# Kernel optimization log

Measured on AMD Instinct MI355X. Metric: run time of the kernel, lower is better.

The kernel has to match this reference:

```python
import jax, jax.numpy as jnp
import numpy as np

D_MODEL = 128
SEQ_LEN = 2048
WINDOW = 64
BATCH = 32


def setup_inputs() -> dict:
    key = jax.random.key(0)
    ks = jax.random.split(key, 6)
    scale = 1.0 / np.sqrt(D_MODEL)
    return {
        "x": jax.random.normal(ks[0], (BATCH, D_MODEL, SEQ_LEN), dtype=jnp.float32),
        "Wq": jax.random.normal(ks[1], (D_MODEL, D_MODEL), dtype=jnp.float32) * scale,
        "bq": jnp.zeros((D_MODEL,), dtype=jnp.float32),
        "Wk": jax.random.normal(ks[2], (D_MODEL, D_MODEL), dtype=jnp.float32) * scale,
        "bk": jnp.zeros((D_MODEL,), dtype=jnp.float32),
        "Wv": jax.random.normal(ks[3], (D_MODEL, D_MODEL), dtype=jnp.float32) * scale,
        "bv": jnp.zeros((D_MODEL,), dtype=jnp.float32),
        "Wo": jax.random.normal(ks[4], (D_MODEL, D_MODEL), dtype=jnp.float32) * scale,
        "bo": jnp.zeros((D_MODEL,), dtype=jnp.float32),
        "pos_bias": jax.random.normal(ks[5], (SEQ_LEN, SEQ_LEN), dtype=jnp.float32) * 0.02,
    }


def reference(x, Wq, bq, Wk, bk, Wv, bv, Wo, bo, pos_bias):
    # x: [N, C, L] -> [N, L, C]  (in_proj Rearrange)
    xt = jnp.swapaxes(x, 1, 2)
    L = xt.shape[1]

    q = xt @ Wq + bq  # [N, L, d]
    k = xt @ Wk + bk
    v = xt @ Wv + bv

    # AFT-Local positional bias: w_{t,t'} = pos_bias if |t-t'| < s else 0
    idx = jnp.arange(L)
    local_mask = (jnp.abs(idx[:, None] - idx[None, :]) < WINDOW).astype(xt.dtype)
    pb = pos_bias[:L, :L] * local_mask  # [L, L]

    # numerically stable exponentials (AFT paper / labml formulation)
    exp_k = jnp.exp(k - jnp.max(k, axis=1, keepdims=True))          # [N, L, d]
    exp_pb = jnp.exp(pb - jnp.max(pb, axis=1, keepdims=True))       # [L, L]

    num = jnp.einsum('ij,njd->nid', exp_pb, exp_k * v)  # [N, L, d]
    den = jnp.einsum('ij,njd->nid', exp_pb, exp_k)      # [N, L, d]

    y = jax.nn.sigmoid(q) * num / den
    out = y @ Wo + bo  # output projection

    # out_proj Rearrange: [N, L, C] -> [N, C, L]
    return jnp.swapaxes(out, 1, 2)
```

## Files before the change

### kernel.cpp

```cpp
#include <hip/hip_runtime.h>
#include <math.h>

#define NB 32
#define DM 128
#define SL 2048
#define WIN 64
#define NT  (SL / 16)
#define PADF 4
#define PADB 6
#define NTP (NT + PADF + PADB)
#define YST 132
#define NSEG 64

typedef __attribute__((ext_vector_type(8))) short bf16x8;
typedef __attribute__((ext_vector_type(8))) unsigned short u16x8;
typedef __attribute__((ext_vector_type(4))) float f32x4;

__device__ inline ushort bf16_rne(float f) {
    union { float f; unsigned u; } v; v.f = f;
    unsigned u = v.u;
    return (ushort)((u + 0x7FFFu + ((u >> 16) & 1u)) >> 16);
}
__device__ inline float bf16_to_f(ushort h) {
    union { unsigned u; float f; } v; v.u = ((unsigned)h) << 16;
    return v.f;
}
__device__ inline ushort bf16_hi_trunc(float f) {
    union { float f; unsigned u; } v; v.f = f;
    return (ushort)(v.u >> 16);
}


__global__ __launch_bounds__(512) void setup_kernel(
    const float* __restrict__ Wq, const float* __restrict__ Wk,
    const float* __restrict__ Wv, const float* __restrict__ Wo,
    const float* __restrict__ pos_bias,
    ushort* __restrict__ Wh, ushort* __restrict__ Wl,
    ushort* __restrict__ WB)
{
    const int b = blockIdx.x;
    const int tid = threadIdx.x;
    if (b < 128) {
        const int id = b;
        const int mat = id >> 5;
        const int ct = (id & 31) >> 2, ks = id & 3;
        const int lane = tid >> 3, j = tid & 7;
        const int k = ks * 32 + (lane >> 4) * 8 + j;
        const int col = ct * 16 + (lane & 15);
        const float* W = (mat == 0) ? Wq : ((mat == 1) ? Wk : ((mat == 2) ? Wv : Wo));
        float w = W[k * DM + col];
        ushort h = bf16_rne(w);
        Wh[(size_t)id * 512 + tid] = h;
        Wl[(size_t)id * 512 + tid] = bf16_rne(w - bf16_to_f(h));
    } else {
        const int idx = b - 128;
        const int it = idx >> 1;
        const int half = idx & 1;
        const int i0 = it * 16;
        const int tend = half * 1280 + 1280;
        for (int t = half * 1280 + tid; t < tend; t += 512) {
            const int ks = t >> 9;
            const int lane = (t >> 3) & 63;
            const int jj = t & 7;
            const int m = lane & 15;
            const int k = ks * 32 + ((lane >> 4) << 3) + jj;
            const int i = i0 + m;
            const int j = i0 - 64 + k;
            const int rel = k - 64 - m;
            float val = 0.f;
            if (rel > -WIN && rel < WIN && j >= 0 && j < SL)
                val = __expf(pos_bias[(size_t)i * SL + j]) - 1.f;
            WB[(size_t)it * 2560 + t] = bf16_rne(val);
        }
    }
}

__global__ __launch_bounds__(512, 6) void qkv_kernel(
    const float* __restrict__ x,
    const ushort* __restrict__ Wh, const ushort* __restrict__ Wl,
    const float* __restrict__ bq, const float* __restrict__ bk,
    const float* __restrict__ bv,
    ushort* __restrict__ sqh, ushort* __restrict__ ekTF, ushort* __restrict__ ekvTF,
    float* __restrict__ Pk, float* __restrict__ Pkv)
{
    __shared__ ushort Ah[32 * 128];
    __shared__ ushort Al[32 * 128];
    const int n = blockIdx.y, bx = blockIdx.x, l0 = bx * 32;
    const int tid = threadIdx.x;
    const int wave = tid >> 6;
    const int lane = tid & 63;

    if (bx < 10) {
        const int jt_p = (bx < PADF) ? bx : (NT + bx);
        const size_t zb = ((size_t)n * NTP + jt_p) * 2048 + (size_t)tid * 4;
        ushort4 z; z.x = 0; z.y = 0; z.z = 0; z.w = 0;
        *(ushort4*)&ekTF [zb] = z;
        *(ushort4*)&ekvTF[zb] = z;
    }

    {
        const int lo = tid & 31;
        const int cq = tid >> 5;
        const int l  = l0 + lo;
        const int c0 = cq * 8;
        float xv[8];
        #pragma unroll
        for (int u = 0; u < 8; ++u)
            xv[u] = x[((size_t)n * DM + c0 + u) * SL + l];
        u16x8 hv, lv;
        #pragma unroll
        for (int u = 0; u < 8; ++u) {
            const ushort h = bf16_hi_trunc(xv[u]);
            hv[u] = h;
            lv[u] = bf16_rne(xv[u] - bf16_to_f(h));
        }
        const int lt = lo >> 4, m = lo & 15;
        const int ks = cq >> 2, oct = cq & 3;
        const int idx = ((lt * 4 + ks) * 64 + oct * 16 + m) * 8;
        *(u16x8*)&Ah[idx] = hv;
        *(u16x8*)&Al[idx] = lv;
    }
    __syncthreads();

    const int dcol = lane & 15;
    const int d = wave * 16 + dcol;

    f32x4 acc[3][2];
    {
        const float b0 = bq[d], b1 = bk[d], b2 = bv[d];
        #pragma unroll
        for (int lt = 0; lt < 2; ++lt) {
            acc[0][lt] = (f32x4){b0, b0, b0, b0};
            acc[1][lt] = (f32x4){b1, b1, b1, b1};
            acc[2][lt] = (f32x4){b2, b2, b2, b2};
        }
    }

    const bf16x8* WhV = (const bf16x8*)Wh;
    const bf16x8* WlV = (const bf16x8*)Wl;
    #pragma unroll
    for (int ks = 0; ks < 4; ++ks) {
        bf16x8 bh[3], bl[3];
        #pragma unroll
        for (int m = 0; m < 3; ++m) {
            const int fi = ((m * 8 + wave) * 4 + ks) * 64 + lane;
            bh[m] = WhV[fi];
            bl[m] = WlV[fi];
        }
        #pragma unroll
        for (int lt = 0; lt < 2; ++lt) {
            const bf16x8 ah = *(const bf16x8*)&Ah[((lt * 4 + ks) * 64 + lane) * 8];
            const bf16x8 al = *(const bf16x8*)&Al[((lt * 4 + ks) * 64 + lane) * 8];
            #pragma unroll
            for (int m = 0; m < 3; ++m) {
                acc[m][lt] = __builtin_amdgcn_mfma_f32_16x16x32_bf16(
                    ah, bh[m], acc[m][lt], 0, 0, 0);
                acc[m][lt] = __builtin_amdgcn_mfma_f32_16x16x32_bf16(
                    al, bh[m], acc[m][lt], 0, 0, 0);
                acc[m][lt] = __builtin_amdgcn_mfma_f32_16x16x32_bf16(
                    ah, bl[m], acc[m][lt], 0, 0, 0);
            }
        }
    }

    const int lrow0 = (lane >> 4) * 4;
    float psk = 0.f, pskv = 0.f;
    #pragma unroll
    for (int lt = 0; lt < 2; ++lt) {
        const f32x4 q4 = acc[0][lt];
        const f32x4 k4 = acc[1][lt];
        const f32x4 v4 = acc[2][lt];
        ushort eh[4], zh[4];
        #pragma unroll
        for (int r = 0; r < 4; ++r) {
            const int l = l0 + lt * 16 + lrow0 + r;
            const float e = __expf(k4[r]);
            const float z = e * v4[r];
            const float s = fminf(__builtin_amdgcn_rcpf(1.f + __expf(-q4[r])), 1.f);
            sqh[((size_t)n * SL + l) * DM + d] = (ushort)(s * 65535.f + 0.5f);
            eh[r] = bf16_rne(e);
            zh[r] = bf16_rne(z);
            psk  += e;
            pskv += z;
        }
        const size_t tb = ((size_t)n * NTP + PADF + (bx * 2 + lt)) * 2048
                        + (size_t)d * 16 + lrow0;
        ushort4 ev; ev.x = eh[0]; ev.y = eh[1]; ev.z = eh[2]; ev.w = eh[3];
        ushort4 zv; zv.x = zh[0]; zv.y = zh[1]; zv.z = zh[2]; zv.w = zh[3];
        *(ushort4*)&ekTF [tb] = ev;
        *(ushort4*)&ekvTF[tb] = zv;
    }
    {
        float a = psk, b = pskv;
        a += __shfl_xor(a, 16, 64); a += __shfl_xor(a, 32, 64);
        b += __shfl_xor(b, 16, 64); b += __shfl_xor(b, 32, 64);
        if (lane < 16) {
            const size_t o = ((size_t)n * NSEG + bx) * DM + d;
            Pk [o] = a;
            Pkv[o] = b;
        }
    }
}

__global__ __launch_bounds__(256, 4) void band_out_kernel(
    const ushort* __restrict__ ekTF, const ushort* __restrict__ ekvTF,
    const ushort* __restrict__ WB,
    const float* __restrict__ Pk, const float* __restrict__ Pkv,
    const ushort* __restrict__ sqg,
    const ushort* __restrict__ Wh, const ushort* __restrict__ Wl,
    const float* __restrict__ bo, float* __restrict__ out)
{
    __shared__ __align__(16) union {
        float ylds[64 * YST];
        float ot[128 * 65];
    } u;
    __shared__ float SkL[DM], SkvL[DM];

    const int bid = blockIdx.x;
    const int xcd = bid & 7;
    const int slot = bid >> 3;
    const int nsub = slot >> 5;
    const int itg  = slot & 31;
    const int n = xcd * 4 + nsub;
    const int wave = threadIdx.x >> 6;
    const int lane = threadIdx.x & 63;
    const int it = itg * 4 + wave;
    const int i0 = it * 16;
    const int l0 = itg * 64;

    const int dcol = lane & 15;
    const int jgrp8 = (lane >> 4) << 3;

    const bf16x8* WBv = (const bf16x8*)(WB + (size_t)it * 2560);
    bf16x8 aWB[5];
    #pragma unroll
    for (int ks = 0; ks < 5; ++ks) aWB[ks] = WBv[ks * 64 + lane];

    {
        const int tdd = threadIdx.x & 127;
        const float* P = (threadIdx.x < 128) ? Pk : Pkv;
        float s = 0.f;
        #pragma unroll
        for (int seg = 0; seg < NSEG; ++seg)
            s += P[((size_t)n * NSEG + seg) * DM + tdd];
        if (threadIdx.x < 128) SkL[tdd] = s; else SkvL[tdd] = s;
    }
    __syncthreads();

    f32x4 den[8], num[8];
    #pragma unroll
    for (int dt = 0; dt < 8; ++dt) {
        const float sk = SkL [dt * 16 + dcol];
        const float sv = SkvL[dt * 16 + dcol];
        den[dt] = (f32x4){sk, sk, sk, sk};
        num[dt] = (f32x4){sv, sv, sv, sv};
    }

    const size_t lsel = (size_t)(lane >> 5) * 2048 + (size_t)((lane >> 4) & 1) * 8
                      + (size_t)dcol * 16;
    #pragma unroll
    for (int ks = 0; ks < 5; ++ks) {
        const bf16x8 a = aWB[ks];
        const size_t tb = ((size_t)n * NTP + it + 2 * ks) * 2048 + lsel;
        #pragma unroll
        for (int dt = 0; dt < 8; ++dt) {
            const size_t rbase = tb + (size_t)dt * 256;
            const bf16x8 bden = *(const bf16x8*)(ekTF  + rbase);
            const bf16x8 bnum = *(const bf16x8*)(ekvTF + rbase);
            den[dt] = __builtin_amdgcn_mfma_f32_16x16x32_bf16(a, bden, den[dt], 0, 0, 0);
            num[dt] = __builtin_amdgcn_mfma_f32_16x16x32_bf16(a, bnum, num[dt], 0, 0, 0);
        }
    }

    const int irow0 = (lane >> 4) << 2;
    #pragma unroll
    for (int dt = 0; dt < 8; ++dt) {
        const int d = dt * 16 + dcol;
        #pragma unroll
        for (int r = 0; r < 4; ++r) {
            const int i = i0 + irow0 + r;
            const float s = (float)sqg[((size_t)n * SL + i) * DM + d] * (1.f / 65535.f);
            const float y = s * num[dt][r] * __builtin_amdgcn_rcpf(den[dt][r]);
            u.ylds[(wave * 16 + irow0 + r) * YST + d] = y;
        }
    }

    bf16x8 yh[4], yl[4];
    {
        const int arow = wave * 16 + (lane & 15);
        #pragma unroll
        for (int ks = 0; ks < 4; ++ks) {
            const int base = arow * YST + ks * 32 + jgrp8;
            const float4 a0 = *(const float4*)&u.ylds[base];
            const float4 a1 = *(const float4*)&u.ylds[base + 4];
            float af[8];
            af[0] = a0.x; af[1] = a0.y; af[2] = a0.z; af[3] = a0.w;
            af[4] = a1.x; af[5] = a1.y; af[6] = a1.z; af[7] = a1.w;
            #pragma unroll
            for (int t = 0; t < 8; ++t) {
                const ushort h = bf16_hi_trunc(af[t]);
                yh[ks][t] = (short)h;
                yl[ks][t] = (short)bf16_rne(af[t] - bf16_to_f(h));
            }
        }
    }
    __syncthreads();

    f32x4 acc[8];
    #pragma unroll
    for (int ct = 0; ct < 8; ++ct) {
        const float b0 = bo[ct * 16 + dcol];
        acc[ct] = (f32x4){b0, b0, b0, b0};
    }

    const bf16x8* WhV = (const bf16x8*)Wh;
    const bf16x8* WlV = (const bf16x8*)Wl;
    #pragma unroll
    for (int ks = 0; ks < 4; ++ks) {
        #pragma unroll
        for (int ct = 0; ct < 8; ++ct) {
            const int fi = ((24 + ct) * 4 + ks) * 64 + lane;
            const bf16x8 bh = WhV[fi];
            const bf16x8 bl = WlV[fi];
            acc[ct] = __builtin_amdgcn_mfma_f32_16x16x32_bf16(yh[ks], bh, acc[ct], 0, 0, 0);
            acc[ct] = __builtin_amdgcn_mfma_f32_16x16x32_bf16(yl[ks], bh, acc[ct], 0, 0, 0);
            acc[ct] = __builtin_amdgcn_mfma_f32_16x16x32_bf16(yh[ks], bl, acc[ct], 0, 0, 0);
        }
    }

    #pragma unroll
    for (int ct = 0; ct < 8; ++ct) {
        const int c = ct * 16 + dcol;
        #pragma unroll
        for (int r = 0; r < 4; ++r)
            u.ot[c * 65 + wave * 16 + irow0 + r] = acc[ct][r];
    }
    __syncthreads();

    const int tid = threadIdx.x;
    #pragma unroll
    for (int rep = 0; rep < 32; ++rep) {
        const int e = rep * 256 + tid;
        const int c = e >> 6, l = e & 63;
        out[((size_t)n * DM + c) * SL + l0 + l] = u.ot[c * 65 + l];
    }
}

extern "C" void kernel_launch(void* const* d_in, const int* in_sizes, int n_in,
                              void* d_out, int out_size, void* d_ws, size_t ws_size,
                              hipStream_t stream)
{
    const float* x        = (const float*)d_in[0];
    const float* Wq       = (const float*)d_in[1];
    const float* bq       = (const float*)d_in[2];
    const float* Wk       = (const float*)d_in[3];
    const float* bk       = (const float*)d_in[4];
    const float* Wv       = (const float*)d_in[5];
    const float* bv       = (const float*)d_in[6];
    const float* Wo       = (const float*)d_in[7];
    const float* bo       = (const float*)d_in[8];
    const float* pos_bias = (const float*)d_in[9];
    float* out = (float*)d_out;

    const size_t NLD = (size_t)NB * SL * DM;
    ushort* sqh   = (ushort*)d_ws;
    ushort* ekTF  = sqh   + NLD;
    ushort* ekvTF = ekTF  + (size_t)NB * NTP * 2048;
    ushort* WB    = ekvTF + (size_t)NB * NTP * 2048;
    float*  Pk    = (float*)(WB + (size_t)128 * 2560);
    float*  Pkv   = Pk   + (size_t)NB * NSEG * DM;
    ushort* Wh    = (ushort*)(Pkv + (size_t)NB * NSEG * DM);
    ushort* Wl    = Wh + (size_t)4 * DM * DM;

    setup_kernel   <<<dim3(384),      512, 0, stream>>>(Wq, Wk, Wv, Wo, pos_bias,
                                                        Wh, Wl, WB);
    qkv_kernel     <<<dim3(NSEG, NB), 512, 0, stream>>>(x, Wh, Wl, bq, bk, bv,
                                                        sqh, ekTF, ekvTF, Pk, Pkv);
    band_out_kernel<<<dim3(NB * 32),  256, 0, stream>>>(ekTF, ekvTF, WB, Pk, Pkv, sqh,
                                                        Wh, Wl, bo, out);
}
```

Measured before the change: 160.0 us.

## Store sigmoid gate in tiled layout and vectorize output stores

```diff
diff --git a/kernel.cpp b/kernel.cpp
--- a/kernel.cpp
+++ b/kernel.cpp
@@ -10,6 +10,7 @@
 #define PADB 6
 #define NTP (NT + PADF + PADB)
 #define YST 132
+#define OST 68
 #define NSEG 64
 
 typedef __attribute__((ext_vector_type(8))) short bf16x8;
@@ -80,7 +81,7 @@
     const ushort* __restrict__ Wh, const ushort* __restrict__ Wl,
     const float* __restrict__ bq, const float* __restrict__ bk,
     const float* __restrict__ bv,
-    ushort* __restrict__ sqh, ushort* __restrict__ ekTF, ushort* __restrict__ ekvTF,
+    ushort* __restrict__ sqT, ushort* __restrict__ ekTF, ushort* __restrict__ ekvTF,
     float* __restrict__ Pk, float* __restrict__ Pkv)
 {
     __shared__ ushort Ah[32 * 128];
@@ -170,25 +171,29 @@
         const f32x4 q4 = acc[0][lt];
         const f32x4 k4 = acc[1][lt];
         const f32x4 v4 = acc[2][lt];
-        ushort eh[4], zh[4];
+        ushort eh[4], zh[4], sh[4];
         #pragma unroll
         for (int r = 0; r < 4; ++r) {
-            const int l = l0 + lt * 16 + lrow0 + r;
             const float e = __expf(k4[r]);
             const float z = e * v4[r];
             const float s = fminf(__builtin_amdgcn_rcpf(1.f + __expf(-q4[r])), 1.f);
-            sqh[((size_t)n * SL + l) * DM + d] = (ushort)(s * 65535.f + 0.5f);
+            sh[r] = (ushort)(s * 65535.f + 0.5f);
             eh[r] = bf16_rne(e);
             zh[r] = bf16_rne(z);
             psk  += e;
             pskv += z;
         }
-        const size_t tb = ((size_t)n * NTP + PADF + (bx * 2 + lt)) * 2048
+        const int jt = bx * 2 + lt;
+        const size_t tb = ((size_t)n * NTP + PADF + jt) * 2048
+                        + (size_t)d * 16 + lrow0;
+        const size_t sb = ((size_t)n * NT + jt) * 2048
                         + (size_t)d * 16 + lrow0;
         ushort4 ev; ev.x = eh[0]; ev.y = eh[1]; ev.z = eh[2]; ev.w = eh[3];
         ushort4 zv; zv.x = zh[0]; zv.y = zh[1]; zv.z = zh[2]; zv.w = zh[3];
+        ushort4 sv; sv.x = sh[0]; sv.y = sh[1]; sv.z = sh[2]; sv.w = sh[3];
         *(ushort4*)&ekTF [tb] = ev;
         *(ushort4*)&ekvTF[tb] = zv;
+        *(ushort4*)&sqT  [sb] = sv;
     }
     {
         float a = psk, b = pskv;
@@ -206,13 +211,13 @@
     const ushort* __restrict__ ekTF, const ushort* __restrict__ ekvTF,
     const ushort* __restrict__ WB,
     const float* __restrict__ Pk, const float* __restrict__ Pkv,
-    const ushort* __restrict__ sqg,
+    const ushort* __restrict__ sqT,
     const ushort* __restrict__ Wh, const ushort* __restrict__ Wl,
     const float* __restrict__ bo, float* __restrict__ out)
 {
     __shared__ __align__(16) union {
         float ylds[64 * YST];
-        float ot[128 * 65];
+        float ot[128 * OST];
     } u;
     __shared__ float SkL[DM], SkvL[DM];
 
@@ -225,7 +230,6 @@
     const int wave = threadIdx.x >> 6;
     const int lane = threadIdx.x & 63;
     const int it = itg * 4 + wave;
-    const int i0 = it * 16;
     const int l0 = itg * 64;
 
     const int dcol = lane & 15;
@@ -273,13 +277,17 @@
     }
 
     const int irow0 = (lane >> 4) << 2;
+    const size_t sgb = ((size_t)n * NT + it) * 2048 + irow0;
     #pragma unroll
     for (int dt = 0; dt < 8; ++dt) {
         const int d = dt * 16 + dcol;
+        const ushort4 s4 = *(const ushort4*)&sqT[sgb + (size_t)d * 16];
+        float sf[4];
+        sf[0] = (float)s4.x; sf[1] = (float)s4.y;
+        sf[2] = (float)s4.z; sf[3] = (float)s4.w;
         #pragma unroll
         for (int r = 0; r < 4; ++r) {
-            const int i = i0 + irow0 + r;
-            const float s = (float)sqg[((size_t)n * SL + i) * DM + d] * (1.f / 65535.f);
+            const float s = sf[r] * (1.f / 65535.f);
             const float y = s * num[dt][r] * __builtin_amdgcn_rcpf(den[dt][r]);
             u.ylds[(wave * 16 + irow0 + r) * YST + d] = y;
         }
@@ -333,16 +341,18 @@
         const int c = ct * 16 + dcol;
         #pragma unroll
         for (int r = 0; r < 4; ++r)
-            u.ot[c * 65 + wave * 16 + irow0 + r] = acc[ct][r];
+            u.ot[c * OST + wave * 16 + irow0 + r] = acc[ct][r];
     }
     __syncthreads();
 
     const int tid = threadIdx.x;
     #pragma unroll
-    for (int rep = 0; rep < 32; ++rep) {
+    for (int rep = 0; rep < 8; ++rep) {
         const int e = rep * 256 + tid;
-        const int c = e >> 6, l = e & 63;
-        out[((size_t)n * DM + c) * SL + l0 + l] = u.ot[c * 65 + l];
+        const int c = e >> 4;
+        const int lq = e & 15;
+        const float4 v = *(const float4*)&u.ot[c * OST + lq * 4];
+        *(float4*)&out[((size_t)n * DM + c) * SL + l0 + lq * 4] = v;
     }
 }
 
@@ -362,9 +372,8 @@
     const float* pos_bias = (const float*)d_in[9];
     float* out = (float*)d_out;
 
-    const size_t NLD = (size_t)NB * SL * DM;
-    ushort* sqh   = (ushort*)d_ws;
-    ushort* ekTF  = sqh   + NLD;
+    ushort* sqT   = (ushort*)d_ws;
+    ushort* ekTF  = sqT   + (size_t)NB * NT * 2048;
     ushort* ekvTF = ekTF  + (size_t)NB * NTP * 2048;
     ushort* WB    = ekvTF + (size_t)NB * NTP * 2048;
     float*  Pk    = (float*)(WB + (size_t)128 * 2560);
@@ -375,7 +384,7 @@
     setup_kernel   <<<dim3(384),      512, 0, stream>>>(Wq, Wk, Wv, Wo, pos_bias,
                                                         Wh, Wl, WB);
     qkv_kernel     <<<dim3(NSEG, NB), 512, 0, stream>>>(x, Wh, Wl, bq, bk, bv,
-                                                        sqh, ekTF, ekvTF, Pk, Pkv);
-    band_out_kernel<<<dim3(NB * 32),  256, 0, stream>>>(ekTF, ekvTF, WB, Pk, Pkv, sqh,
+                                                        sqT, ekTF, ekvTF, Pk, Pkv);
+    band_out_kernel<<<dim3(NB * 32),  256, 0, stream>>>(ekTF, ekvTF, WB, Pk, Pkv, sqT,
                                                         Wh, Wl, bo, out);
 }
```

New measurement: 160.3 us. Within noise of the previous version (+0.2%).
